# Performance work log

Measured on AMD Instinct MI355X. Metric: run time of the kernel, lower is better.

Reference implementation:

```python
import jax, jax.numpy as jnp
import numpy as np

N_ATOMS = 100_000
N_BONDS = 200_000
MAX_NB = 6
ATOM_FDIM = 133
BOND_FDIM = 147
HIDDEN = 256
DEPTH = 5
ATOMS_PER_MOL = 100


def setup_inputs() -> dict:
    key = jax.random.key(0)
    ks = jax.random.split(key, 9)
    f_atoms = jax.random.normal(ks[0], (N_ATOMS, ATOM_FDIM), dtype=jnp.float32)
    f_bonds = jax.random.normal(ks[1], (N_BONDS, BOND_FDIM), dtype=jnp.float32)
    a2b = jax.random.randint(ks[2], (N_ATOMS, MAX_NB), 0, N_BONDS, dtype=jnp.int32)
    b2a = jax.random.randint(ks[3], (N_BONDS,), 0, N_ATOMS, dtype=jnp.int32)
    # reverse bond of 2i is 2i+1 and vice versa (chemprop directed-bond pairing)
    b2revb = (jnp.arange(N_BONDS, dtype=jnp.int32) ^ 1)
    s_i = 1.0 / np.sqrt(BOND_FDIM)
    s_h = 1.0 / np.sqrt(HIDDEN)
    s_o = 1.0 / np.sqrt(ATOM_FDIM + HIDDEN)
    W_i = jax.random.uniform(ks[4], (HIDDEN, BOND_FDIM), jnp.float32, -s_i, s_i)
    W_h = jax.random.uniform(ks[5], (HIDDEN, HIDDEN), jnp.float32, -s_h, s_h)
    W_o = jax.random.uniform(ks[6], (HIDDEN, ATOM_FDIM + HIDDEN), jnp.float32, -s_o, s_o)
    b_o = jax.random.uniform(ks[7], (HIDDEN,), jnp.float32, -s_o, s_o)
    return {"f_atoms": f_atoms, "f_bonds": f_bonds, "a2b": a2b, "b2a": b2a,
            "b2revb": b2revb, "W_i": W_i, "W_h": W_h, "W_o": W_o, "b_o": b_o,
            "atoms_per_mol": ATOMS_PER_MOL}


def reference(f_atoms, f_bonds, a2b, b2a, b2revb, W_i, W_h, W_o, b_o, atoms_per_mol):
    # input = W_i(f_bonds); message = relu(input)   [n_bonds, H]
    inp = jnp.einsum('bf,hf->bh', f_bonds, W_i)
    message = jax.nn.relu(inp)
    for _ in range(DEPTH - 1):
        # gather incoming-bond messages per atom and sum: [n_atoms, max_nb, H] -> [n_atoms, H]
        a_message = message[a2b].sum(axis=1)
        # directed-MPNN update: subtract reverse-bond message
        m = a_message[b2a] - message[b2revb]
        message = jax.nn.relu(inp + jnp.einsum('bh,gh->bg', m, W_h))
        # dropout p=0.0 (eval) -> identity
    a_message = message[a2b].sum(axis=1)                      # [n_atoms, H]
    a_input = jnp.concatenate([f_atoms, a_message], axis=1)   # [n_atoms, atom_fdim+H]
    atom_hiddens = jax.nn.relu(jnp.einsum('af,hf->ah', a_input, W_o) + b_o)
    # uniform a_scope: stack per-molecule atom blocks -> [n_mols, atoms_per_mol, H]
    return atom_hiddens.reshape(-1, atoms_per_mol, HIDDEN)
```

## Files before the change

### kernel.cpp

```cpp
#include <hip/hip_runtime.h>
#include <hip/hip_bf16.h>

typedef unsigned short u16;
typedef short s8vec __attribute__((ext_vector_type(8)));
typedef float f4vec __attribute__((ext_vector_type(4)));

__device__ __forceinline__ float bf2f(u16 u) {
    union { unsigned int i; float f; } c; c.i = ((unsigned int)u) << 16; return c.f;
}
__device__ __forceinline__ u16 f2bf(float f) {
    union { float f; unsigned int i; } c; c.f = f;
    unsigned int x = c.i;
    x += 0x7fffu + ((x >> 16) & 1u);
    return (u16)(x >> 16);
}

__device__ __forceinline__ void gload_lds16(const void* g, void* l) {
    __builtin_amdgcn_global_load_lds((__attribute__((address_space(1))) void*)g,
                                     (__attribute__((address_space(3))) void*)l, 16, 0, 0);
}

__global__ void pad_cvt_kernel(const float* __restrict__ src, u16* __restrict__ dst,
                               int rows, int scol, int dcol) {
    for (int r = blockIdx.x; r < rows; r += gridDim.x) {
        for (int c = threadIdx.x; c < dcol; c += 256) {
            float v = (c < scol) ? src[(size_t)r * scol + c] : 0.f;
            dst[(size_t)r * dcol + c] = f2bf(v);
        }
    }
}

__global__ void build_ain_kernel(const float* __restrict__ f_atoms, const u16* __restrict__ amsg,
                                 u16* __restrict__ dst, int rows) {
    for (int r = blockIdx.x; r < rows; r += gridDim.x) {
        for (int c = threadIdx.x; c < 448; c += 256) {
            float v;
            if (c < 133)      v = f_atoms[(size_t)r * 133 + c];
            else if (c < 389) v = bf2f(amsg[(size_t)r * 256 + (c - 133)]);
            else              v = 0.f;
            dst[(size_t)r * 448 + c] = f2bf(v);
        }
    }
}

__global__ void gather6_kernel(const u16* __restrict__ P, const int* __restrict__ a2b,
                               u16* __restrict__ out, int n_atoms) {
    int lane = threadIdx.x & 63;
    int wid = (blockIdx.x * blockDim.x + threadIdx.x) >> 6;
    int nw = (gridDim.x * blockDim.x) >> 6;
    for (int a = wid; a < n_atoms; a += nw) {
        float a0 = 0.f, a1 = 0.f, a2 = 0.f, a3 = 0.f;
#pragma unroll
        for (int j = 0; j < 6; ++j) {
            int b = a2b[a * 6 + j];
            ushort4 v = *(const ushort4*)(P + (size_t)b * 256 + lane * 4);
            a0 += bf2f(v.x); a1 += bf2f(v.y); a2 += bf2f(v.z); a3 += bf2f(v.w);
        }
        ushort4 o; o.x = f2bf(a0); o.y = f2bf(a1); o.z = f2bf(a2); o.w = f2bf(a3);
        *(ushort4*)(out + (size_t)a * 256 + lane * 4) = o;
    }
}

__global__ void update_kernel(const u16* __restrict__ inp, const u16* __restrict__ aP,
                              const u16* __restrict__ P, const int* __restrict__ b2a,
                              const int* __restrict__ b2revb, u16* __restrict__ msg, int n_bonds) {
    int lane = threadIdx.x & 63;
    int wid = (blockIdx.x * blockDim.x + threadIdx.x) >> 6;
    int nw = (gridDim.x * blockDim.x) >> 6;
    for (int b = wid; b < n_bonds; b += nw) {
        int a = b2a[b];
        int rb = b2revb[b];
        ushort4 vi = *(const ushort4*)(inp + (size_t)b * 256 + lane * 4);
        ushort4 va = *(const ushort4*)(aP + (size_t)a * 256 + lane * 4);
        ushort4 vp = *(const ushort4*)(P + (size_t)rb * 256 + lane * 4);
        ushort4 o;
        o.x = f2bf(fmaxf(bf2f(vi.x) + bf2f(va.x) - bf2f(vp.x), 0.f));
        o.y = f2bf(fmaxf(bf2f(vi.y) + bf2f(va.y) - bf2f(vp.y), 0.f));
        o.z = f2bf(fmaxf(bf2f(vi.z) + bf2f(va.z) - bf2f(vp.z), 0.f));
        o.w = f2bf(fmaxf(bf2f(vi.w) + bf2f(va.w) - bf2f(vp.w), 0.f));
        *(ushort4*)(msg + (size_t)b * 256 + lane * 4) = o;
    }
}

template <int EPI>
__launch_bounds__(256, 2)
__global__ void gemm_kernel(const u16* __restrict__ A, const u16* __restrict__ B,
                            int M, int Kp, int nk,
                            void* __restrict__ out0, void* __restrict__ out1,
                            const float* __restrict__ bias) {
    __shared__ __align__(16) char smem[2][2][16384];
    const int t = threadIdx.x;
    const int w = t >> 6, lane = t & 63;
    const int row0 = blockIdx.x * 128;
    const int col0 = blockIdx.y * 128;
    const int wm = w >> 1, wn = w & 1;

    f4vec acc[4][4];
#pragma unroll
    for (int i = 0; i < 4; ++i)
#pragma unroll
        for (int j = 0; j < 4; ++j) acc[i][j] = (f4vec){0.f, 0.f, 0.f, 0.f};

    auto stage = [&](int buf, int k0) {
#pragma unroll
        for (int i = 0; i < 4; ++i) {
            int rlin = (w * 4 + i) * 8 + (lane >> 3);
            int slot = lane & 7;
            int chunk = slot ^ (rlin & 7);
            int grow = row0 + rlin; if (grow >= M) grow = M - 1;
            const u16* gp = A + (size_t)grow * Kp + k0 + chunk * 8;
            gload_lds16(gp, &smem[buf][0][(w * 4 + i) * 1024]);
        }
#pragma unroll
        for (int i = 0; i < 4; ++i) {
            int rlin = (w * 4 + i) * 8 + (lane >> 3);
            int slot = lane & 7;
            int chunk = slot ^ (rlin & 7);
            const u16* gp = B + (size_t)(col0 + rlin) * Kp + k0 + chunk * 8;
            gload_lds16(gp, &smem[buf][1][(w * 4 + i) * 1024]);
        }
    };

    auto compute = [&](int buf) {
#pragma unroll
        for (int kk = 0; kk < 2; ++kk) {
            s8vec af[4], bfr[4];
#pragma unroll
            for (int i = 0; i < 4; ++i) {
                int r = wm * 64 + i * 16 + (lane & 15);
                int chunk = (kk * 4 + (lane >> 4)) ^ (r & 7);
                af[i] = *(const s8vec*)&smem[buf][0][r * 128 + chunk * 16];
            }
#pragma unroll
            for (int j = 0; j < 4; ++j) {
                int c = wn * 64 + j * 16 + (lane & 15);
                int chunk = (kk * 4 + (lane >> 4)) ^ (c & 7);
                bfr[j] = *(const s8vec*)&smem[buf][1][c * 128 + chunk * 16];
            }
#pragma unroll
            for (int i = 0; i < 4; ++i)
#pragma unroll
                for (int j = 0; j < 4; ++j)
                    acc[i][j] = __builtin_amdgcn_mfma_f32_16x16x32_bf16(af[i], bfr[j], acc[i][j], 0, 0, 0);
        }
    };

    stage(0, 0);
    __syncthreads();
    int cur = 0;
    for (int ks = 0; ks < nk; ++ks) {
        if (ks + 1 < nk) stage(cur ^ 1, (ks + 1) * 64);
        compute(cur);
        __syncthreads();
        cur ^= 1;
    }

#pragma unroll
    for (int i = 0; i < 4; ++i) {
        int Rbase = row0 + wm * 64 + i * 16 + (lane >> 4) * 4;
#pragma unroll
        for (int j = 0; j < 4; ++j) {
            int C = col0 + wn * 64 + j * 16 + (lane & 15);
#pragma unroll
            for (int r = 0; r < 4; ++r) {
                int R = Rbase + r;
                if (R < M) {
                    float v = acc[i][j][r];
                    if (EPI == 0) {
                        ((u16*)out0)[(size_t)R * 256 + C] = f2bf(v);
                        ((u16*)out1)[(size_t)R * 256 + C] = f2bf(fmaxf(v, 0.f));
                    } else if (EPI == 1) {
                        ((u16*)out0)[(size_t)R * 256 + C] = f2bf(v);
                    } else {
                        ((float*)out0)[(size_t)R * 256 + C] = fmaxf(v + bias[C], 0.f);
                    }
                }
            }
        }
    }
}

extern "C" void kernel_launch(void* const* d_in, const int* in_sizes, int n_in,
                              void* d_out, int out_size, void* d_ws, size_t ws_size,
                              hipStream_t stream) {
    const float* f_atoms = (const float*)d_in[0];
    const float* f_bonds = (const float*)d_in[1];
    const int* a2b = (const int*)d_in[2];
    const int* b2a = (const int*)d_in[3];
    const int* b2revb = (const int*)d_in[4];
    const float* W_i = (const float*)d_in[5];
    const float* W_h = (const float*)d_in[6];
    const float* W_o = (const float*)d_in[7];
    const float* b_o = (const float*)d_in[8];

    const int NA = 100000, NB = 200000;

    char* ws = (char*)d_ws;
    u16* fb  = (u16*)(ws + 0);
    u16* inp = (u16*)(ws + 76800000);
    u16* msg = (u16*)(ws + 179200000);
    u16* P   = (u16*)(ws + 281600000);
    u16* aP  = (u16*)(ws + 384000000);
    u16* Wi  = (u16*)(ws + 435200000);
    u16* Wh  = (u16*)(ws + 435298304);
    u16* Wo  = (u16*)(ws + 435429376);
    u16* ain = (u16*)(ws + 0);
    if (ws_size < 435658752u) return;

    pad_cvt_kernel<<<dim3(8192), dim3(256), 0, stream>>>(f_bonds, fb, NB, 147, 192);
    pad_cvt_kernel<<<dim3(256), dim3(256), 0, stream>>>(W_i, Wi, 256, 147, 192);
    pad_cvt_kernel<<<dim3(256), dim3(256), 0, stream>>>(W_h, Wh, 256, 256, 256);
    pad_cvt_kernel<<<dim3(256), dim3(256), 0, stream>>>(W_o, Wo, 256, 389, 448);

    gemm_kernel<0><<<dim3(1563, 2), dim3(256), 0, stream>>>(fb, Wi, NB, 192, 3, inp, msg, nullptr);

    for (int it = 0; it < 4; ++it) {
        gemm_kernel<1><<<dim3(1563, 2), dim3(256), 0, stream>>>(msg, Wh, NB, 256, 4, P, nullptr, nullptr);
        gather6_kernel<<<dim3(25000), dim3(256), 0, stream>>>(P, a2b, aP, NA);
        update_kernel<<<dim3(50000), dim3(256), 0, stream>>>(inp, aP, P, b2a, b2revb, msg, NB);
    }

    gather6_kernel<<<dim3(25000), dim3(256), 0, stream>>>(msg, a2b, aP, NA);
    build_ain_kernel<<<dim3(8192), dim3(256), 0, stream>>>(f_atoms, aP, ain, NA);
    gemm_kernel<2><<<dim3(782, 2), dim3(256), 0, stream>>>(ain, Wo, NA, 448, 7, d_out, nullptr, b_o);
}
```

Before: 1.038 ms.

## Fuse bond update into GEMM staging and push weights before gathers

Removes the separate update, padding and concat kernels by computing relu(inp + aP[b2a] - P[b^1]) directly while staging the A tile of the W_h GEMM. Weights are applied before the per-atom gather, so the final W_o projection is split: one part goes through the bond messages, and f_atoms is handled in a small GEMM with the gathered term added in its epilogue. The GEMM now covers all 256 output columns per block with 512 threads, and the gather uses 8-wide vector loads. The cost is register-staged A loads instead of async LDS loads, plus reliance on the b^1 reverse-bond pairing.

```diff
diff --git a/kernel.cpp b/kernel.cpp
--- a/kernel.cpp
+++ b/kernel.cpp
@@ -2,6 +2,7 @@
 #include <hip/hip_bf16.h>
 
 typedef unsigned short u16;
+typedef unsigned short u16x8 __attribute__((ext_vector_type(8)));
 typedef short s8vec __attribute__((ext_vector_type(8)));
 typedef float f4vec __attribute__((ext_vector_type(4)));
 
@@ -20,80 +21,53 @@
                                      (__attribute__((address_space(3))) void*)l, 16, 0, 0);
 }
 
-__global__ void pad_cvt_kernel(const float* __restrict__ src, u16* __restrict__ dst,
-                               int rows, int scol, int dcol) {
-    for (int r = blockIdx.x; r < rows; r += gridDim.x) {
-        for (int c = threadIdx.x; c < dcol; c += 256) {
-            float v = (c < scol) ? src[(size_t)r * scol + c] : 0.f;
-            dst[(size_t)r * dcol + c] = f2bf(v);
-        }
-    }
-}
-
-__global__ void build_ain_kernel(const float* __restrict__ f_atoms, const u16* __restrict__ amsg,
-                                 u16* __restrict__ dst, int rows) {
-    for (int r = blockIdx.x; r < rows; r += gridDim.x) {
-        for (int c = threadIdx.x; c < 448; c += 256) {
-            float v;
-            if (c < 133)      v = f_atoms[(size_t)r * 133 + c];
-            else if (c < 389) v = bf2f(amsg[(size_t)r * 256 + (c - 133)]);
-            else              v = 0.f;
-            dst[(size_t)r * 448 + c] = f2bf(v);
-        }
+__global__ void pad_w_kernel(const float* __restrict__ src, u16* __restrict__ dst,
+                             int sstride, int col0, int nvalid, int dcol) {
+    int r = blockIdx.x;
+    for (int c = threadIdx.x; c < dcol; c += blockDim.x) {
+        float v = (c < nvalid) ? src[(size_t)r * sstride + col0 + c] : 0.f;
+        dst[(size_t)r * dcol + c] = f2bf(v);
     }
 }
 
 __global__ void gather6_kernel(const u16* __restrict__ P, const int* __restrict__ a2b,
                                u16* __restrict__ out, int n_atoms) {
     int lane = threadIdx.x & 63;
+    int half = lane >> 5;
+    int col = (lane & 31) * 8;
     int wid = (blockIdx.x * blockDim.x + threadIdx.x) >> 6;
     int nw = (gridDim.x * blockDim.x) >> 6;
-    for (int a = wid; a < n_atoms; a += nw) {
-        float a0 = 0.f, a1 = 0.f, a2 = 0.f, a3 = 0.f;
+    for (int a0 = wid * 2; a0 < n_atoms; a0 += nw * 2) {
+        int a = a0 + half;
+        float acc[8];
+#pragma unroll
+        for (int e = 0; e < 8; ++e) acc[e] = 0.f;
 #pragma unroll
         for (int j = 0; j < 6; ++j) {
             int b = a2b[a * 6 + j];
-            ushort4 v = *(const ushort4*)(P + (size_t)b * 256 + lane * 4);
-            a0 += bf2f(v.x); a1 += bf2f(v.y); a2 += bf2f(v.z); a3 += bf2f(v.w);
-        }
-        ushort4 o; o.x = f2bf(a0); o.y = f2bf(a1); o.z = f2bf(a2); o.w = f2bf(a3);
-        *(ushort4*)(out + (size_t)a * 256 + lane * 4) = o;
-    }
-}
-
-__global__ void update_kernel(const u16* __restrict__ inp, const u16* __restrict__ aP,
-                              const u16* __restrict__ P, const int* __restrict__ b2a,
-                              const int* __restrict__ b2revb, u16* __restrict__ msg, int n_bonds) {
-    int lane = threadIdx.x & 63;
-    int wid = (blockIdx.x * blockDim.x + threadIdx.x) >> 6;
-    int nw = (gridDim.x * blockDim.x) >> 6;
-    for (int b = wid; b < n_bonds; b += nw) {
-        int a = b2a[b];
-        int rb = b2revb[b];
-        ushort4 vi = *(const ushort4*)(inp + (size_t)b * 256 + lane * 4);
-        ushort4 va = *(const ushort4*)(aP + (size_t)a * 256 + lane * 4);
-        ushort4 vp = *(const ushort4*)(P + (size_t)rb * 256 + lane * 4);
-        ushort4 o;
-        o.x = f2bf(fmaxf(bf2f(vi.x) + bf2f(va.x) - bf2f(vp.x), 0.f));
-        o.y = f2bf(fmaxf(bf2f(vi.y) + bf2f(va.y) - bf2f(vp.y), 0.f));
-        o.z = f2bf(fmaxf(bf2f(vi.z) + bf2f(va.z) - bf2f(vp.z), 0.f));
-        o.w = f2bf(fmaxf(bf2f(vi.w) + bf2f(va.w) - bf2f(vp.w), 0.f));
-        *(ushort4*)(msg + (size_t)b * 256 + lane * 4) = o;
-    }
-}
-
-template <int EPI>
-__launch_bounds__(256, 2)
-__global__ void gemm_kernel(const u16* __restrict__ A, const u16* __restrict__ B,
-                            int M, int Kp, int nk,
-                            void* __restrict__ out0, void* __restrict__ out1,
-                            const float* __restrict__ bias) {
-    __shared__ __align__(16) char smem[2][2][16384];
+            u16x8 v = *(const u16x8*)(P + (size_t)b * 256 + col);
+#pragma unroll
+            for (int e = 0; e < 8; ++e) acc[e] += bf2f(v[e]);
+        }
+        u16x8 o;
+#pragma unroll
+        for (int e = 0; e < 8; ++e) o[e] = f2bf(acc[e]);
+        *(u16x8*)(out + (size_t)a * 256 + col) = o;
+    }
+}
+
+template <int ASTAGE, int EPI>
+__launch_bounds__(512, 2)
+__global__ void gemm256_kernel(const void* __restrict__ Asrc, const u16* __restrict__ Pm,
+                               const u16* __restrict__ aPm, const int* __restrict__ b2a,
+                               const u16* __restrict__ B, int M, int Kp, int scol, int nk,
+                               void* __restrict__ out0, const u16* __restrict__ aQ,
+                               const float* __restrict__ bias) {
+    __shared__ __align__(16) char smem[2][49152];
     const int t = threadIdx.x;
     const int w = t >> 6, lane = t & 63;
     const int row0 = blockIdx.x * 128;
-    const int col0 = blockIdx.y * 128;
-    const int wm = w >> 1, wn = w & 1;
+    const int wm = w >> 2, wn = w & 3;
 
     f4vec acc[4][4];
 #pragma unroll
@@ -107,17 +81,39 @@
             int rlin = (w * 4 + i) * 8 + (lane >> 3);
             int slot = lane & 7;
             int chunk = slot ^ (rlin & 7);
-            int grow = row0 + rlin; if (grow >= M) grow = M - 1;
-            const u16* gp = A + (size_t)grow * Kp + k0 + chunk * 8;
-            gload_lds16(gp, &smem[buf][0][(w * 4 + i) * 1024]);
-        }
-#pragma unroll
-        for (int i = 0; i < 4; ++i) {
-            int rlin = (w * 4 + i) * 8 + (lane >> 3);
-            int slot = lane & 7;
-            int chunk = slot ^ (rlin & 7);
-            const u16* gp = B + (size_t)(col0 + rlin) * Kp + k0 + chunk * 8;
-            gload_lds16(gp, &smem[buf][1][(w * 4 + i) * 1024]);
+            const u16* gp = B + (size_t)rlin * Kp + k0 + chunk * 8;
+            gload_lds16(gp, &smem[buf][16384 + (w * 4 + i) * 1024]);
+        }
+#pragma unroll
+        for (int i = 0; i < 2; ++i) {
+            int cid = t * 2 + i;
+            int r = cid >> 3, slot = cid & 7;
+            int grow = row0 + r; if (grow >= M) grow = M - 1;
+            int coff = k0 + slot * 8;
+            u16x8 v;
+            if (ASTAGE == 1) {
+                const float* src = (const float*)Asrc + (size_t)grow * scol;
+#pragma unroll
+                for (int e = 0; e < 8; ++e) {
+                    int c = coff + e;
+                    v[e] = (c < scol) ? f2bf(src[c]) : (u16)0;
+                }
+            } else if (ASTAGE == 2) {
+                u16x8 x = *(const u16x8*)((const u16*)Asrc + (size_t)grow * 256 + coff);
+#pragma unroll
+                for (int e = 0; e < 8; ++e) v[e] = (x[e] >> 15) ? (u16)0 : x[e];
+            } else {
+                int pr = grow ^ 1;
+                int a = b2a[grow];
+                u16x8 vi = *(const u16x8*)((const u16*)Asrc + (size_t)grow * 256 + coff);
+                u16x8 vp = *(const u16x8*)(Pm + (size_t)pr * 256 + coff);
+                u16x8 va = *(const u16x8*)(aPm + (size_t)a * 256 + coff);
+#pragma unroll
+                for (int e = 0; e < 8; ++e)
+                    v[e] = f2bf(fmaxf(bf2f(vi[e]) + bf2f(va[e]) - bf2f(vp[e]), 0.f));
+            }
+            int chunk = slot ^ (r & 7);
+            *(u16x8*)&smem[buf][r * 128 + chunk * 16] = v;
         }
     };
 
@@ -129,13 +125,13 @@
             for (int i = 0; i < 4; ++i) {
                 int r = wm * 64 + i * 16 + (lane & 15);
                 int chunk = (kk * 4 + (lane >> 4)) ^ (r & 7);
-                af[i] = *(const s8vec*)&smem[buf][0][r * 128 + chunk * 16];
+                af[i] = *(const s8vec*)&smem[buf][r * 128 + chunk * 16];
             }
 #pragma unroll
             for (int j = 0; j < 4; ++j) {
                 int c = wn * 64 + j * 16 + (lane & 15);
                 int chunk = (kk * 4 + (lane >> 4)) ^ (c & 7);
-                bfr[j] = *(const s8vec*)&smem[buf][1][c * 128 + chunk * 16];
+                bfr[j] = *(const s8vec*)&smem[buf][16384 + c * 128 + chunk * 16];
             }
 #pragma unroll
             for (int i = 0; i < 4; ++i)
@@ -160,7 +156,7 @@
         int Rbase = row0 + wm * 64 + i * 16 + (lane >> 4) * 4;
 #pragma unroll
         for (int j = 0; j < 4; ++j) {
-            int C = col0 + wn * 64 + j * 16 + (lane & 15);
+            int C = wn * 64 + j * 16 + (lane & 15);
 #pragma unroll
             for (int r = 0; r < 4; ++r) {
                 int R = Rbase + r;
@@ -168,11 +164,9 @@
                     float v = acc[i][j][r];
                     if (EPI == 0) {
                         ((u16*)out0)[(size_t)R * 256 + C] = f2bf(v);
-                        ((u16*)out1)[(size_t)R * 256 + C] = f2bf(fmaxf(v, 0.f));
-                    } else if (EPI == 1) {
-                        ((u16*)out0)[(size_t)R * 256 + C] = f2bf(v);
                     } else {
-                        ((float*)out0)[(size_t)R * 256 + C] = fmaxf(v + bias[C], 0.f);
+                        float o = v + bf2f(aQ[(size_t)R * 256 + C]) + bias[C];
+                        ((float*)out0)[(size_t)R * 256 + C] = fmaxf(o, 0.f);
                     }
                 }
             }
@@ -187,7 +181,6 @@
     const float* f_bonds = (const float*)d_in[1];
     const int* a2b = (const int*)d_in[2];
     const int* b2a = (const int*)d_in[3];
-    const int* b2revb = (const int*)d_in[4];
     const float* W_i = (const float*)d_in[5];
     const float* W_h = (const float*)d_in[6];
     const float* W_o = (const float*)d_in[7];
@@ -196,31 +189,43 @@
     const int NA = 100000, NB = 200000;
 
     char* ws = (char*)d_ws;
-    u16* fb  = (u16*)(ws + 0);
-    u16* inp = (u16*)(ws + 76800000);
-    u16* msg = (u16*)(ws + 179200000);
-    u16* P   = (u16*)(ws + 281600000);
-    u16* aP  = (u16*)(ws + 384000000);
-    u16* Wi  = (u16*)(ws + 435200000);
-    u16* Wh  = (u16*)(ws + 435298304);
-    u16* Wo  = (u16*)(ws + 435429376);
-    u16* ain = (u16*)(ws + 0);
-    if (ws_size < 435658752u) return;
-
-    pad_cvt_kernel<<<dim3(8192), dim3(256), 0, stream>>>(f_bonds, fb, NB, 147, 192);
-    pad_cvt_kernel<<<dim3(256), dim3(256), 0, stream>>>(W_i, Wi, 256, 147, 192);
-    pad_cvt_kernel<<<dim3(256), dim3(256), 0, stream>>>(W_h, Wh, 256, 256, 256);
-    pad_cvt_kernel<<<dim3(256), dim3(256), 0, stream>>>(W_o, Wo, 256, 389, 448);
-
-    gemm_kernel<0><<<dim3(1563, 2), dim3(256), 0, stream>>>(fb, Wi, NB, 192, 3, inp, msg, nullptr);
-
-    for (int it = 0; it < 4; ++it) {
-        gemm_kernel<1><<<dim3(1563, 2), dim3(256), 0, stream>>>(msg, Wh, NB, 256, 4, P, nullptr, nullptr);
-        gather6_kernel<<<dim3(25000), dim3(256), 0, stream>>>(P, a2b, aP, NA);
-        update_kernel<<<dim3(50000), dim3(256), 0, stream>>>(inp, aP, P, b2a, b2revb, msg, NB);
-    }
-
-    gather6_kernel<<<dim3(25000), dim3(256), 0, stream>>>(msg, a2b, aP, NA);
-    build_ain_kernel<<<dim3(8192), dim3(256), 0, stream>>>(f_atoms, aP, ain, NA);
-    gemm_kernel<2><<<dim3(782, 2), dim3(256), 0, stream>>>(ain, Wo, NA, 448, 7, d_out, nullptr, b_o);
-}
+    u16* inp = (u16*)(ws + 0);
+    u16* Pa  = (u16*)(ws + 102400000);
+    u16* Pb  = (u16*)(ws + 204800000);
+    u16* aP  = (u16*)(ws + 307200000);
+    u16* Wi  = (u16*)(ws + 358400000);
+    u16* Wh  = (u16*)(ws + 358498304);
+    u16* Wo2 = (u16*)(ws + 358629376);
+    u16* Wo1 = (u16*)(ws + 358760448);
+    if (ws_size < 358858752u) return;
+
+    pad_w_kernel<<<dim3(256), dim3(256), 0, stream>>>(W_i, Wi, 147, 0, 147, 192);
+    pad_w_kernel<<<dim3(256), dim3(256), 0, stream>>>(W_h, Wh, 256, 0, 256, 256);
+    pad_w_kernel<<<dim3(256), dim3(256), 0, stream>>>(W_o, Wo2, 389, 133, 256, 256);
+    pad_w_kernel<<<dim3(256), dim3(256), 0, stream>>>(W_o, Wo1, 389, 0, 133, 192);
+
+    const int GB = (NB + 127) / 128;
+    const int GA = (NA + 127) / 128;
+
+    gemm256_kernel<1, 0><<<dim3(GB), dim3(512), 0, stream>>>(
+        f_bonds, nullptr, nullptr, nullptr, Wi, NB, 192, 147, 3, inp, nullptr, nullptr);
+
+    gemm256_kernel<2, 0><<<dim3(GB), dim3(512), 0, stream>>>(
+        inp, nullptr, nullptr, nullptr, Wh, NB, 256, 0, 4, Pa, nullptr, nullptr);
+    gather6_kernel<<<dim3(2048), dim3(256), 0, stream>>>(Pa, a2b, aP, NA);
+
+    u16* Pcur = Pa; u16* Pnxt = Pb;
+    for (int it = 0; it < 3; ++it) {
+        gemm256_kernel<4, 0><<<dim3(GB), dim3(512), 0, stream>>>(
+            inp, Pcur, aP, b2a, Wh, NB, 256, 0, 4, Pnxt, nullptr, nullptr);
+        gather6_kernel<<<dim3(2048), dim3(256), 0, stream>>>(Pnxt, a2b, aP, NA);
+        u16* tmp = Pcur; Pcur = Pnxt; Pnxt = tmp;
+    }
+
+    gemm256_kernel<4, 0><<<dim3(GB), dim3(512), 0, stream>>>(
+        inp, Pcur, aP, b2a, Wo2, NB, 256, 0, 4, Pnxt, nullptr, nullptr);
+    gather6_kernel<<<dim3(2048), dim3(256), 0, stream>>>(Pnxt, a2b, aP, NA);
+
+    gemm256_kernel<1, 3><<<dim3(GA), dim3(512), 0, stream>>>(
+        f_atoms, nullptr, nullptr, nullptr, Wo1, NA, 192, 133, 3, d_out, aP, b_o);
+}
```

New measurement: 1.034 ms. About the same (-0.4%).
